# Kernel optimization log

Hardware: AMD Instinct MI355X
Metric: run time of the kernel (lower is better)

## Reference

```python
import jax, jax.numpy as jnp
import numpy as np

B, D = 256, 8                 # trees, tree depth (leaves at level D)
V, E, H = 32000, 128, 128     # vocab, embedding_dim, hidden_dim
N = 2 ** (D + 1) - 1          # 511 heap-indexed nodes per tree


def setup_inputs() -> dict:
    key = jax.random.key(0)
    ks = jax.random.split(key, 9)
    s = 0.05  # keep gate pre-activations in a sane range
    return {
        "tokens": jax.random.randint(ks[0], (B, N), 0, V),
        "arity": jax.random.randint(ks[1], (B, 2 ** D - 1), 0, 2).astype(jnp.int32),
        "emb": jax.random.normal(ks[2], (V, E), dtype=jnp.float32) * s,
        "W": jax.random.normal(ks[3], (4, E, H), dtype=jnp.float32) * s,      # i,f,o,u
        "bW": jax.random.normal(ks[4], (4, H), dtype=jnp.float32) * s,
        "Ubin": jax.random.normal(ks[5], (5, 2 * H, H), dtype=jnp.float32) * s,  # i,f_l,f_r,o,u
        "bUbin": jax.random.normal(ks[6], (5, H), dtype=jnp.float32) * s,
        "Uun": jax.random.normal(ks[7], (4, H, H), dtype=jnp.float32) * s,    # i,f,o,u
        "bUun": jax.random.normal(ks[8], (4, H), dtype=jnp.float32) * s,
    }


def reference(tokens, arity, emb, W, bW, Ubin, bUbin, Uun, bUun):
    # Level-synchronous bottom-up Tree-LSTM over heap-indexed perfect trees.
    x = emb[tokens]  # [B, N, E] embedding gather for every node
    depth = int(np.log2(tokens.shape[1] + 1)) - 1

    # Leaves (level `depth`): h = tanh(W_u x + b_u), c = 0
    off = 2 ** depth - 1
    lx = x[:, off:]  # [B, 2^D, E]
    h = jnp.tanh(jnp.einsum('bne,eh->bnh', lx, W[3]) + bW[3])
    c = jnp.zeros_like(h)

    for l in range(depth - 1, -1, -1):
        o2, cnt = 2 ** l - 1, 2 ** l
        nx = x[:, o2:o2 + cnt]            # [B, cnt, E] this level's tokens
        h_l, h_r = h[:, ::2], h[:, 1::2]   # children (heap order)
        c_l, c_r = c[:, ::2], c[:, 1::2]

        # Shared input projections for all 4 gates, fused into one GEMM
        Wx = jnp.einsum('bne,geh->gbnh', nx, W) + bW[:, None, None, :]
        hcat = jnp.concatenate([h_l, h_r], axis=-1)  # [B, cnt, 2H]
        Ub = jnp.einsum('bnk,gkh->gbnh', hcat, Ubin) + bUbin[:, None, None, :]
        Uu = jnp.einsum('bnh,gha->gbna', h_l, Uun) + bUun[:, None, None, :]

        # Binary branch: i, f_l, f_r (shared W_f), o, u
        i_b = jax.nn.sigmoid(Wx[0] + Ub[0])
        f_lg = jax.nn.sigmoid(Wx[1] + Ub[1])
        f_rg = jax.nn.sigmoid(Wx[1] + Ub[2])
        o_b = jax.nn.sigmoid(Wx[2] + Ub[3])
        u_b = jnp.tanh(Wx[3] + Ub[4])
        c_b = i_b * u_b + f_lg * c_l + f_rg * c_r
        h_b = o_b * jnp.tanh(c_b)

        # Unary branch (child = left child)
        i_u = jax.nn.sigmoid(Wx[0] + Uu[0])
        f_u = jax.nn.sigmoid(Wx[1] + Uu[1])
        o_u = jax.nn.sigmoid(Wx[2] + Uu[2])
        u_u = jnp.tanh(Wx[3] + Uu[3])
        c_u = i_u * u_u + f_u * c_l
        h_u = o_u * jnp.tanh(c_u)

        m = (arity[:, o2:o2 + cnt] == 1)[..., None]  # True -> binary node
        h = jnp.where(m, h_b, h_u)
        c = jnp.where(m, c_b, c_u)

    return h[:, 0], c[:, 0]  # root (h, c), each [B, H]
```

## Files before the change

### kernel.cpp

```cpp
#include <hip/hip_runtime.h>
#include <hip/hip_bf16.h>

#define NTOK 511
#define NINT 255

typedef unsigned short u16;
typedef __attribute__((ext_vector_type(8))) short bf16x8;
typedef __attribute__((ext_vector_type(4))) float f32x4;

constexpr int OFF_FLAG = 0;
constexpr int OFF_WB   = 4;
constexpr int W3B = 294912;
constexpr int WB_ELEMS = 311296;
constexpr int OFF_BIAS = OFF_WB + WB_ELEMS / 2;
constexpr int BW4 = 0, BUB4 = 512, BUB1 = 1024, BUU4 = 1152, B3 = 1664;
constexpr int BIAS_FLOATS = 1792;
constexpr int OFF_ROOT  = OFF_BIAS + BIAS_FLOATS;
constexpr int OFF_CHUNK = OFF_ROOT + 65536;
constexpr long PER_TREE = 49152;

__device__ __forceinline__ float bf2f(__hip_bfloat16 v) { return __bfloat162float(v); }
__device__ __forceinline__ short f2s(float f) {
    __hip_bfloat16 b = __float2bfloat16(f);
    return *reinterpret_cast<short*>(&b);
}
__device__ __forceinline__ float sigm(float x) { return 1.0f / (1.0f + __expf(-x)); }
__device__ __forceinline__ float tanh_(float x) { return 1.0f - 2.0f / (__expf(2.0f * x) + 1.0f); }

__device__ __forceinline__ float ldf(const void* p, long idx, int isbf) {
    return isbf ? bf2f(((const __hip_bfloat16*)p)[idx]) : ((const float*)p)[idx];
}

__device__ __forceinline__ bf16x8 ldA(const void* p, long idx, int isbf) {
    if (isbf) return *(const bf16x8*)((const short*)p + idx);
    const float* f = (const float*)p + idx;
    float4 a = *(const float4*)f, b = *(const float4*)(f + 4);
    bf16x8 r;
    r[0] = f2s(a.x); r[1] = f2s(a.y); r[2] = f2s(a.z); r[3] = f2s(a.w);
    r[4] = f2s(b.x); r[5] = f2s(b.y); r[6] = f2s(b.z); r[7] = f2s(b.w);
    return r;
}

typedef const __attribute__((address_space(1))) unsigned int* gp1_t;
typedef __attribute__((address_space(3))) unsigned int* lp3_t;
__device__ __forceinline__ void stage16(const void* g, void* l) {
    __builtin_amdgcn_global_load_lds((gp1_t)g, (lp3_t)l, 16, 0, 0);
}
__device__ __forceinline__ void stage36(const short* g, short* l, int t) {
#pragma unroll
    for (int s = 0; s < 9; ++s) {
        int off = (s * 256 + t) * 8;
        stage16(g + off, l + off);
    }
}

__global__ void detect_kernel(const void* W, float* ws) {
    if (threadIdx.x == 0 && blockIdx.x == 0) {
        const u16* u = (const u16*)W;
        int cnt = 0;
        for (int i = 0; i < 128; i += 2) {
            u16 x = u[i];
            int ex = (x >> 7) & 0xff;
            if (x == 0 || (ex >= 96 && ex <= 127)) cnt++;
        }
        ((int*)ws)[0] = (cnt >= 48) ? 1 : 0;
    }
}

__global__ __launch_bounds__(256) void repack_mfma(
    const void* W, const void* bW, const void* Ubin, const void* bUbin,
    const void* Uun, const void* bUun, float* ws)
{
    const int isbf = ((const int*)ws)[0];
    short* wb = (short*)(ws + OFF_WB);
    float* bias = ws + OFF_BIAS;
    int tid = blockIdx.x * blockDim.x + threadIdx.x;
    int nth = gridDim.x * blockDim.x;

    for (int idx = tid; idx < 294912; idx += nth) {
        int e = idx & 511, fjc = idx >> 9;
        int jc = fjc / 72, f = fjc - jc * 72;
        int lane = e >> 3, id8 = e & 7;
        int j = jc * 16 + (lane & 15);
        float v;
        if (f < 16) {
            int g = f >> 2, ks = f & 3;
            int k = ks * 32 + (lane >> 4) * 8 + id8;
            v = ldf(W, (long)g * 16384 + k * 128 + j, isbf);
        } else if (f < 32) {
            int fu = f - 16; int g = fu >> 2, ks = fu & 3;
            int k = ks * 32 + (lane >> 4) * 8 + id8;
            v = ldf(Uun, (long)g * 16384 + k * 128 + j, isbf);
        } else {
            int fb = f - 32; int g = fb >> 3, ks = fb & 7;
            int k = ks * 32 + (lane >> 4) * 8 + id8;
            v = ldf(Ubin, (long)g * 32768 + k * 128 + j, isbf);
        }
        wb[idx] = f2s(v);
    }
    for (int idx = tid; idx < 16384; idx += nth) {
        int e = idx & 511, frag = idx >> 9;
        int jc = frag >> 2, ks = frag & 3;
        int lane = e >> 3, id8 = e & 7;
        int k = ks * 32 + (lane >> 4) * 8 + id8;
        int j = jc * 16 + (lane & 15);
        wb[W3B + idx] = f2s(ldf(W, (long)3 * 16384 + k * 128 + j, isbf));
    }
    for (int j = tid; j < 128; j += nth) {
        float4 b;
        b.x = ldf(bW, 0 * 128 + j, isbf); b.y = ldf(bW, 1 * 128 + j, isbf);
        b.z = ldf(bW, 2 * 128 + j, isbf); b.w = ldf(bW, 3 * 128 + j, isbf);
        ((float4*)(bias + BW4))[j] = b;
        float4 bb;
        bb.x = ldf(bUbin, 0 * 128 + j, isbf); bb.y = ldf(bUbin, 1 * 128 + j, isbf);
        bb.z = ldf(bUbin, 2 * 128 + j, isbf); bb.w = ldf(bUbin, 3 * 128 + j, isbf);
        ((float4*)(bias + BUB4))[j] = bb;
        (bias + BUB1)[j] = ldf(bUbin, 4 * 128 + j, isbf);
        float4 bu;
        bu.x = ldf(bUun, 0 * 128 + j, isbf); bu.y = ldf(bUun, 1 * 128 + j, isbf);
        bu.z = ldf(bUun, 2 * 128 + j, isbf); bu.w = ldf(bUun, 3 * 128 + j, isbf);
        ((float4*)(bias + BUU4))[j] = bu;
        (bias + B3)[j] = ldf(bW, 3 * 128 + j, isbf);
    }
}

#define MFMA(A, B, C) __builtin_amdgcn_mfma_f32_16x16x32_bf16(A, B, C, 0, 0, 0)

__global__ __launch_bounds__(256, 2) void leaf_mfma(
    const int* __restrict__ tokens, const void* emb, const float* __restrict__ ws,
    short* __restrict__ hOut, int treeOff, int Mtot, int iters)
{
    __shared__ short hst[4][16][132];
    const int t = threadIdx.x;
    const int isbf = ((const int*)ws)[0];
    const int wv = t >> 6, lane = t & 63, quad = lane >> 4, l16 = lane & 15;
    const short* wb = (const short*)(ws + OFF_WB);
    const float* bias = ws + OFF_BIAS;

    bf16x8 bf[32];
#pragma unroll
    for (int f = 0; f < 32; ++f)
        bf[f] = *(const bf16x8*)(wb + W3B + f * 512 + lane * 8);
    float b3v[8];
#pragma unroll
    for (int jc = 0; jc < 8; ++jc) b3v[jc] = (bias + B3)[jc * 16 + l16];

    for (int it = 0; it < iters; ++it) {
        int rb = (blockIdx.x * iters + it) * 64 + wv * 16;
        if (rb >= Mtot) break;
        int p = rb + l16; if (p >= Mtot) p = Mtot - 1;
        int bl = p >> 8, i = p & 255;
        int tk = tokens[(long)(treeOff + bl) * NTOK + 255 + i];
        bf16x8 ax[4];
#pragma unroll
        for (int ks = 0; ks < 4; ++ks)
            ax[ks] = ldA(emb, (long)tk * 128 + ks * 32 + quad * 8, isbf);
        f32x4 acc[8];
#pragma unroll
        for (int jc = 0; jc < 8; ++jc) acc[jc] = {0.f, 0.f, 0.f, 0.f};
#pragma unroll
        for (int jc = 0; jc < 8; ++jc)
#pragma unroll
            for (int ks = 0; ks < 4; ++ks)
                acc[jc] = MFMA(ax[ks], bf[jc * 4 + ks], acc[jc]);
#pragma unroll
        for (int jc = 0; jc < 8; ++jc)
#pragma unroll
            for (int r = 0; r < 4; ++r)
                hst[wv][quad * 4 + r][jc * 16 + l16] = f2s(tanh_(acc[jc][r] + b3v[jc]));
        int nloc = lane >> 2, c0 = (lane & 3) * 4;
        int prow = rb + nloc;
        if (prow < Mtot) {
#pragma unroll
            for (int jcb = 0; jcb < 8; ++jcb) {
                uint2 v = *(const uint2*)&hst[wv][nloc][jcb * 16 + c0];
                *(uint2*)&hOut[((long)jcb * Mtot + prow) * 16 + c0] = v;
            }
        }
    }
}

template <int JCC, int MT>
__global__ __launch_bounds__(256, 2) void level_mfma(
    const int* __restrict__ tokens, const int* __restrict__ arity, const void* emb,
    const float* __restrict__ ws, const short* __restrict__ hChild,
    const float* __restrict__ cChild, short* __restrict__ hOut, float* __restrict__ cOut,
    float* __restrict__ rootH, float* __restrict__ rootC,
    int lvl, int treeOff, int leafchild, int isRoot, int Mtot, int Mchild, int NBM)
{
    __shared__ short Bs0[36 * 512];
    __shared__ short Bs1[36 * 512];
    __shared__ short hst[4][MT][16][20];
    __shared__ int tok[64 * MT];
    __shared__ int ar[64 * MT];

    constexpr int NODES = 64 * MT;
    const int t = threadIdx.x;
    const int isbf = ((const int*)ws)[0];
    const int jsx = blockIdx.x / NBM;
    const int mb  = blockIdx.x - jsx * NBM;
    const int jcLo = jsx * JCC;
    const int p0 = mb * NODES;
    const int wv = t >> 6, lane = t & 63, quad = lane >> 4, l16 = lane & 15;
    const int cnt = 1 << lvl, o2 = cnt - 1;
    const short* wb = (const short*)(ws + OFF_WB);
    const float* bias = ws + OFF_BIAS;

    if (t < NODES) {
        int p = p0 + t; if (p >= Mtot) p = Mtot - 1;
        int bl = p >> lvl, i = p - (bl << lvl);
        tok[t] = tokens[(long)(treeOff + bl) * NTOK + o2 + i];
        ar[t]  = arity[(long)(treeOff + bl) * NINT + o2 + i];
    }
    stage36(wb + (long)jcLo * 36864, Bs0, t);
    __syncthreads();

    bf16x8 ax[MT][4], ah[MT][8];
#pragma unroll
    for (int mt = 0; mt < MT; ++mt) {
        int row = wv * (16 * MT) + mt * 16 + l16;
        int p = p0 + row; if (p >= Mtot) p = Mtot - 1;
        int bl = p >> lvl, i = p - (bl << lvl);
        long crow = (long)bl * (cnt << 1) + 2 * i;
        int tk = tok[row];
#pragma unroll
        for (int ks = 0; ks < 4; ++ks)
            ax[mt][ks] = ldA(emb, (long)tk * 128 + ks * 32 + quad * 8, isbf);
#pragma unroll
        for (int ks = 0; ks < 8; ++ks) {
            int k0 = ks * 32 + quad * 8;
            int side = k0 >> 7, kl = k0 & 127;
            ah[mt][ks] = *(const bf16x8*)(hChild +
                ((long)(kl >> 4) * Mchild + crow + side) * 16 + (kl & 15));
        }
    }

    for (int jx = 0; jx < JCC; ++jx) {
        const int jc = jcLo + jx;
        const short* wj = wb + (long)jc * 36864;

        stage36(wj + 36 * 512, Bs1, t);

        float clv[MT][4], crv[MT][4];
#pragma unroll
        for (int mt = 0; mt < MT; ++mt)
#pragma unroll
        for (int r = 0; r < 4; ++r) {
            if (!leafchild) {
                int pe = p0 + wv * (16 * MT) + mt * 16 + quad * 4 + r;
                if (pe >= Mtot) pe = Mtot - 1;
                int ble = pe >> lvl, ie = pe - (ble << lvl);
                long crowe = (long)ble * (cnt << 1) + 2 * ie;
                clv[mt][r] = cChild[((long)jc * Mchild + crowe) * 16 + l16];
                crv[mt][r] = cChild[((long)jc * Mchild + crowe + 1) * 16 + l16];
            } else { clv[mt][r] = 0.f; crv[mt][r] = 0.f; }
        }

        const int j = jc * 16 + l16;
        const float4 bw = ((const float4*)(bias + BW4))[j];
        const float4 bb = ((const float4*)(bias + BUB4))[j];
        const float  b1 = (bias + BUB1)[j];
        const float4 bu = ((const float4*)(bias + BUU4))[j];

        f32x4 aW[4][MT], aU[4][MT], aB[5][MT];
#pragma unroll
        for (int g = 0; g < 4; ++g)
#pragma unroll
            for (int mt = 0; mt < MT; ++mt) { aW[g][mt] = {0,0,0,0}; aU[g][mt] = {0,0,0,0}; }
#pragma unroll
        for (int g = 0; g < 5; ++g)
#pragma unroll
            for (int mt = 0; mt < MT; ++mt) aB[g][mt] = {0,0,0,0};

#pragma unroll
        for (int f = 0; f < 16; ++f) {
            bf16x8 b = *(const bf16x8*)&Bs0[f * 512 + lane * 8];
#pragma unroll
            for (int mt = 0; mt < MT; ++mt)
                aW[f >> 2][mt] = MFMA(ax[mt][f & 3], b, aW[f >> 2][mt]);
        }
#pragma unroll
        for (int f = 16; f < 32; ++f) {
            bf16x8 b = *(const bf16x8*)&Bs0[f * 512 + lane * 8];
            int g = (f - 16) >> 2, ks = (f - 16) & 3;
#pragma unroll
            for (int mt = 0; mt < MT; ++mt)
                aU[g][mt] = MFMA(ah[mt][ks], b, aU[g][mt]);
        }
#pragma unroll
        for (int f = 32; f < 36; ++f) {
            bf16x8 b = *(const bf16x8*)&Bs0[f * 512 + lane * 8];
#pragma unroll
            for (int mt = 0; mt < MT; ++mt)
                aB[0][mt] = MFMA(ah[mt][f - 32], b, aB[0][mt]);
        }
        __syncthreads();

        if (jx + 1 < JCC)
            stage36(wj + 72 * 512, Bs0, t);

#pragma unroll
        for (int f = 36; f < 72; ++f) {
            bf16x8 b = *(const bf16x8*)&Bs1[(f - 36) * 512 + lane * 8];
            int fb = f - 32, g = fb >> 3, ks = fb & 7;
#pragma unroll
            for (int mt = 0; mt < MT; ++mt)
                aB[g][mt] = MFMA(ah[mt][ks], b, aB[g][mt]);
        }

#pragma unroll
        for (int mt = 0; mt < MT; ++mt) {
#pragma unroll
            for (int r = 0; r < 4; ++r) {
                int ml = wv * (16 * MT) + mt * 16 + quad * 4 + r;
                int p = p0 + ml;
                bool val = (p < Mtot);
                int pc = val ? p : Mtot - 1;
                int bl = pc >> lvl, i = pc - (bl << lvl);
                bool bin = (ar[ml] == 1);
                float w0 = aW[0][mt][r] + bw.x;
                float w1 = aW[1][mt][r] + bw.y;
                float w2 = aW[2][mt][r] + bw.z;
                float w3 = aW[3][mt][r] + bw.w;
                float pi, pf, po, pu;
                if (bin) { pi = w0 + aB[0][mt][r] + bb.x; pf = w1 + aB[1][mt][r] + bb.y;
                           po = w2 + aB[3][mt][r] + bb.w; pu = w3 + aB[4][mt][r] + b1; }
                else     { pi = w0 + aU[0][mt][r] + bu.x; pf = w1 + aU[1][mt][r] + bu.y;
                           po = w2 + aU[2][mt][r] + bu.z; pu = w3 + aU[3][mt][r] + bu.w; }
                float cl = clv[mt][r];
                float cr = bin ? crv[mt][r] : 0.f;
                float frv = bin ? sigm(w1 + aB[2][mt][r] + bb.z) : 0.f;
                float ig = sigm(pi), fg = sigm(pf), og = sigm(po), ug = tanh_(pu);
                float c = ig * ug + fg * cl + frv * cr;
                float h = og * tanh_(c);
                if (isRoot) {
                    if (val) {
                        rootH[(long)(treeOff + bl) * 128 + j] = h;
                        rootC[(long)(treeOff + bl) * 128 + j] = c;
                    }
                } else {
                    if (val) cOut[((long)jc * Mtot + pc) * 16 + l16] = c;
                    hst[wv][mt][quad * 4 + r][l16] = f2s(h);
                }
            }
        }
        if (!isRoot) {
            int nloc = lane >> 2, c0 = (lane & 3) * 4;
#pragma unroll
            for (int mt = 0; mt < MT; ++mt) {
                int prow = p0 + wv * (16 * MT) + mt * 16 + nloc;
                if (prow < Mtot) {
                    uint2 v = *(const uint2*)&hst[wv][mt][nloc][c0];
                    *(uint2*)&hOut[((long)jc * Mtot + prow) * 16 + c0] = v;
                }
            }
        }
        __syncthreads();
    }
}

__global__ __launch_bounds__(256) void out_kernel(const float* ws, void* out)
{
    const int isbf = ((const int*)ws)[0];
    const float* rootH = ws + OFF_ROOT;
    const float* rootC = rootH + 32768;
    int t = blockIdx.x * 256 + threadIdx.x;
    float h = rootH[t], c = rootC[t];
    if (isbf) {
        ((__hip_bfloat16*)out)[t]         = __float2bfloat16(h);
        ((__hip_bfloat16*)out)[32768 + t] = __float2bfloat16(c);
    } else {
        ((float*)out)[t]         = h;
        ((float*)out)[32768 + t] = c;
    }
}

extern "C" void kernel_launch(void* const* d_in, const int* in_sizes, int n_in,
                              void* d_out, int out_size, void* d_ws, size_t ws_size,
                              hipStream_t stream)
{
    const int* tokens = (const int*)d_in[0];
    const int* arity  = (const int*)d_in[1];
    const void* emb   = d_in[2];
    const void* W     = d_in[3];
    const void* bW    = d_in[4];
    const void* Ubin  = d_in[5];
    const void* bUbin = d_in[6];
    const void* Uun   = d_in[7];
    const void* bUun  = d_in[8];

    float* ws = (float*)d_ws;

    int Bc = 256;
    while (Bc > 1 && (size_t)(OFF_CHUNK + Bc * PER_TREE) * 4 > ws_size) Bc >>= 1;
    const int nCh = 256 / Bc;

    detect_kernel<<<1, 64, 0, stream>>>(W, ws);
    repack_mfma<<<128, 256, 0, stream>>>(W, bW, Ubin, bUbin, Uun, bUun, ws);

    short* Ha = (short*)(ws + OFF_CHUNK);
    short* Hb = Ha + (long)Bc * 32768;
    float* Ca = (float*)(Hb + (long)Bc * 16384);
    float* Cb = Ca + (long)Bc * 8192;
    float* rootH = ws + OFF_ROOT;
    float* rootC = rootH + 32768;

    for (int cidx = 0; cidx < nCh; ++cidx) {
        int toff = cidx * Bc;
        {
            int Mleaf = Bc * 256;
            int NBL = (Mleaf + 63) / 64; if (NBL > 512) NBL = 512;
            int itersL = (Mleaf + NBL * 64 - 1) / (NBL * 64);
            leaf_mfma<<<NBL, 256, 0, stream>>>(tokens, emb, ws, Ha, toff, Mleaf, itersL);
        }
        for (int l = 7; l >= 0; --l) {
            int M = Bc << l;
            int Mchild = Bc << (l + 1);
            const short* hC = (l & 1) ? Ha : Hb;
            const float* cC = (l & 1) ? Ca : Cb;
            short* hO = (l & 1) ? Hb : Ha;
            float* cO = (l & 1) ? Cb : Ca;
            int lc = (l == 7) ? 1 : 0;
            int isRoot = (l == 0) ? 1 : 0;
            if (l >= 5) {
                int Mb = (M + 127) / 128;
                int js = 1;
                while (js < 8 && Mb * js < 512) js <<= 1;
                int jcc = 8 / js;
                dim3 grid(Mb * js);
                if (jcc == 8)
                    level_mfma<8, 2><<<grid, 256, 0, stream>>>(tokens, arity, emb, ws, hC, cC, hO, cO,
                                                               rootH, rootC, l, toff, lc, isRoot, M, Mchild, Mb);
                else if (jcc == 4)
                    level_mfma<4, 2><<<grid, 256, 0, stream>>>(tokens, arity, emb, ws, hC, cC, hO, cO,
                                                               rootH, rootC, l, toff, lc, isRoot, M, Mchild, Mb);
                else if (jcc == 2)
                    level_mfma<2, 2><<<grid, 256, 0, stream>>>(tokens, arity, emb, ws, hC, cC, hO, cO,
                                                               rootH, rootC, l, toff, lc, isRoot, M, Mchild, Mb);
                else
                    level_mfma<1, 2><<<grid, 256, 0, stream>>>(tokens, arity, emb, ws, hC, cC, hO, cO,
                                                               rootH, rootC, l, toff, lc, isRoot, M, Mchild, Mb);
            } else {
                int Mb = (M + 63) / 64;
                dim3 grid(Mb * 8);
                level_mfma<1, 1><<<grid, 256, 0, stream>>>(tokens, arity, emb, ws, hC, cC, hO, cO,
                                                           rootH, rootC, l, toff, lc, isRoot, M, Mchild, Mb);
            }
        }
    }
    out_kernel<<<128, 256, 0, stream>>>(ws, d_out);
}
```

Baseline: 173.8 us.

## Keep one weight column-block resident per workgroup and loop over node tiles

The level kernel is restructured so each workgroup owns a single 16-column output block and stages that block's full 72-fragment weight slice into LDS once. It then loops over Q node tiles, reloading embeddings and child states per tile. Before, each workgroup held its node tile fixed and streamed weight blocks through double-buffered LDS with barriers between them. The change cuts repeated weight staging and the per-iteration syncs, and tokens and arity are now read directly from global memory. In exchange, activations are reloaded for every column block, the larger LDS footprint may lower occupancy, and weight staging no longer overlaps compute.

```diff
diff --git a/kernel.cpp b/kernel.cpp
--- a/kernel.cpp
+++ b/kernel.cpp
@@ -45,13 +45,6 @@
 typedef __attribute__((address_space(3))) unsigned int* lp3_t;
 __device__ __forceinline__ void stage16(const void* g, void* l) {
     __builtin_amdgcn_global_load_lds((gp1_t)g, (lp3_t)l, 16, 0, 0);
-}
-__device__ __forceinline__ void stage36(const short* g, short* l, int t) {
-#pragma unroll
-    for (int s = 0; s < 9; ++s) {
-        int off = (s * 256 + t) * 8;
-        stage16(g + off, l + off);
-    }
 }
 
 __global__ void detect_kernel(const void* W, float* ws) {
@@ -180,88 +173,84 @@
     }
 }
 
-template <int JCC, int MT>
-__global__ __launch_bounds__(256, 2) void level_mfma(
+template <int MT>
+__global__ __launch_bounds__(256, 2) void level2_mfma(
     const int* __restrict__ tokens, const int* __restrict__ arity, const void* emb,
     const float* __restrict__ ws, const short* __restrict__ hChild,
     const float* __restrict__ cChild, short* __restrict__ hOut, float* __restrict__ cOut,
     float* __restrict__ rootH, float* __restrict__ rootC,
-    int lvl, int treeOff, int leafchild, int isRoot, int Mtot, int Mchild, int NBM)
+    int lvl, int treeOff, int leafchild, int isRoot, int Mtot, int Mchild,
+    int NBMB, int Q)
 {
-    __shared__ short Bs0[36 * 512];
-    __shared__ short Bs1[36 * 512];
+    __shared__ short Bs[72 * 512];
     __shared__ short hst[4][MT][16][20];
-    __shared__ int tok[64 * MT];
-    __shared__ int ar[64 * MT];
 
     constexpr int NODES = 64 * MT;
     const int t = threadIdx.x;
     const int isbf = ((const int*)ws)[0];
-    const int jsx = blockIdx.x / NBM;
-    const int mb  = blockIdx.x - jsx * NBM;
-    const int jcLo = jsx * JCC;
-    const int p0 = mb * NODES;
+    const int jc = blockIdx.x / NBMB;
+    const int mb = blockIdx.x - jc * NBMB;
     const int wv = t >> 6, lane = t & 63, quad = lane >> 4, l16 = lane & 15;
     const int cnt = 1 << lvl, o2 = cnt - 1;
     const short* wb = (const short*)(ws + OFF_WB);
     const float* bias = ws + OFF_BIAS;
-
-    if (t < NODES) {
-        int p = p0 + t; if (p >= Mtot) p = Mtot - 1;
-        int bl = p >> lvl, i = p - (bl << lvl);
-        tok[t] = tokens[(long)(treeOff + bl) * NTOK + o2 + i];
-        ar[t]  = arity[(long)(treeOff + bl) * NINT + o2 + i];
-    }
-    stage36(wb + (long)jcLo * 36864, Bs0, t);
+    const short* wj = wb + (long)jc * 36864;
+
+#pragma unroll
+    for (int s = 0; s < 18; ++s) {
+        int off = (s * 256 + t) * 8;
+        stage16(wj + off, Bs + off);
+    }
+
+    const int j = jc * 16 + l16;
+    const float4 bw = ((const float4*)(bias + BW4))[j];
+    const float4 bb = ((const float4*)(bias + BUB4))[j];
+    const float  b1 = (bias + BUB1)[j];
+    const float4 bu = ((const float4*)(bias + BUU4))[j];
+
     __syncthreads();
 
-    bf16x8 ax[MT][4], ah[MT][8];
-#pragma unroll
-    for (int mt = 0; mt < MT; ++mt) {
-        int row = wv * (16 * MT) + mt * 16 + l16;
-        int p = p0 + row; if (p >= Mtot) p = Mtot - 1;
-        int bl = p >> lvl, i = p - (bl << lvl);
-        long crow = (long)bl * (cnt << 1) + 2 * i;
-        int tk = tok[row];
-#pragma unroll
-        for (int ks = 0; ks < 4; ++ks)
-            ax[mt][ks] = ldA(emb, (long)tk * 128 + ks * 32 + quad * 8, isbf);
-#pragma unroll
-        for (int ks = 0; ks < 8; ++ks) {
-            int k0 = ks * 32 + quad * 8;
-            int side = k0 >> 7, kl = k0 & 127;
-            ah[mt][ks] = *(const bf16x8*)(hChild +
-                ((long)(kl >> 4) * Mchild + crow + side) * 16 + (kl & 15));
-        }
-    }
-
-    for (int jx = 0; jx < JCC; ++jx) {
-        const int jc = jcLo + jx;
-        const short* wj = wb + (long)jc * 36864;
-
-        stage36(wj + 36 * 512, Bs1, t);
-
+    for (int q = 0; q < Q; ++q) {
+        const int p0 = (mb * Q + q) * NODES;
+        if (p0 >= Mtot) break;
+
+        bf16x8 ax[MT][4], ah[MT][8];
+#pragma unroll
+        for (int mt = 0; mt < MT; ++mt) {
+            int row = wv * (16 * MT) + mt * 16 + l16;
+            int p = p0 + row; if (p >= Mtot) p = Mtot - 1;
+            int bl = p >> lvl, i = p - (bl << lvl);
+            long crow = (long)bl * (cnt << 1) + 2 * i;
+            int tk = tokens[(long)(treeOff + bl) * NTOK + o2 + i];
+#pragma unroll
+            for (int ks = 0; ks < 4; ++ks)
+                ax[mt][ks] = ldA(emb, (long)tk * 128 + ks * 32 + quad * 8, isbf);
+#pragma unroll
+            for (int ks = 0; ks < 8; ++ks) {
+                int k0 = ks * 32 + quad * 8;
+                int side = k0 >> 7, kl = k0 & 127;
+                ah[mt][ks] = *(const bf16x8*)(hChild +
+                    ((long)(kl >> 4) * Mchild + crow + side) * 16 + (kl & 15));
+            }
+        }
+
+        int arv[MT][4];
         float clv[MT][4], crv[MT][4];
 #pragma unroll
         for (int mt = 0; mt < MT; ++mt)
 #pragma unroll
         for (int r = 0; r < 4; ++r) {
+            int pe = p0 + wv * (16 * MT) + mt * 16 + quad * 4 + r;
+            if (pe >= Mtot) pe = Mtot - 1;
+            int ble = pe >> lvl, ie = pe - (ble << lvl);
+            arv[mt][r] = arity[(long)(treeOff + ble) * NINT + o2 + ie];
             if (!leafchild) {
-                int pe = p0 + wv * (16 * MT) + mt * 16 + quad * 4 + r;
-                if (pe >= Mtot) pe = Mtot - 1;
-                int ble = pe >> lvl, ie = pe - (ble << lvl);
                 long crowe = (long)ble * (cnt << 1) + 2 * ie;
                 clv[mt][r] = cChild[((long)jc * Mchild + crowe) * 16 + l16];
                 crv[mt][r] = cChild[((long)jc * Mchild + crowe + 1) * 16 + l16];
             } else { clv[mt][r] = 0.f; crv[mt][r] = 0.f; }
         }
 
-        const int j = jc * 16 + l16;
-        const float4 bw = ((const float4*)(bias + BW4))[j];
-        const float4 bb = ((const float4*)(bias + BUB4))[j];
-        const float  b1 = (bias + BUB1)[j];
-        const float4 bu = ((const float4*)(bias + BUU4))[j];
-
         f32x4 aW[4][MT], aU[4][MT], aB[5][MT];
 #pragma unroll
         for (int g = 0; g < 4; ++g)
@@ -274,34 +263,22 @@
 
 #pragma unroll
         for (int f = 0; f < 16; ++f) {
-            bf16x8 b = *(const bf16x8*)&Bs0[f * 512 + lane * 8];
+            bf16x8 b = *(const bf16x8*)&Bs[f * 512 + lane * 8];
 #pragma unroll
             for (int mt = 0; mt < MT; ++mt)
                 aW[f >> 2][mt] = MFMA(ax[mt][f & 3], b, aW[f >> 2][mt]);
         }
 #pragma unroll
         for (int f = 16; f < 32; ++f) {
-            bf16x8 b = *(const bf16x8*)&Bs0[f * 512 + lane * 8];
+            bf16x8 b = *(const bf16x8*)&Bs[f * 512 + lane * 8];
             int g = (f - 16) >> 2, ks = (f - 16) & 3;
 #pragma unroll
             for (int mt = 0; mt < MT; ++mt)
                 aU[g][mt] = MFMA(ah[mt][ks], b, aU[g][mt]);
         }
 #pragma unroll
-        for (int f = 32; f < 36; ++f) {
-            bf16x8 b = *(const bf16x8*)&Bs0[f * 512 + lane * 8];
-#pragma unroll
-            for (int mt = 0; mt < MT; ++mt)
-                aB[0][mt] = MFMA(ah[mt][f - 32], b, aB[0][mt]);
-        }
-        __syncthreads();
-
-        if (jx + 1 < JCC)
-            stage36(wj + 72 * 512, Bs0, t);
-
-#pragma unroll
-        for (int f = 36; f < 72; ++f) {
-            bf16x8 b = *(const bf16x8*)&Bs1[(f - 36) * 512 + lane * 8];
+        for (int f = 32; f < 72; ++f) {
+            bf16x8 b = *(const bf16x8*)&Bs[f * 512 + lane * 8];
             int fb = f - 32, g = fb >> 3, ks = fb & 7;
 #pragma unroll
             for (int mt = 0; mt < MT; ++mt)
@@ -316,8 +293,8 @@
                 int p = p0 + ml;
                 bool val = (p < Mtot);
                 int pc = val ? p : Mtot - 1;
-                int bl = pc >> lvl, i = pc - (bl << lvl);
-                bool bin = (ar[ml] == 1);
+                int bl = pc >> lvl;
+                bool bin = (arv[mt][r] == 1);
                 float w0 = aW[0][mt][r] + bw.x;
                 float w1 = aW[1][mt][r] + bw.y;
                 float w2 = aW[2][mt][r] + bw.z;
@@ -355,7 +332,6 @@
                 }
             }
         }
-        __syncthreads();
     }
 }
 
@@ -423,28 +399,17 @@
             int lc = (l == 7) ? 1 : 0;
             int isRoot = (l == 0) ? 1 : 0;
             if (l >= 5) {
-                int Mb = (M + 127) / 128;
-                int js = 1;
-                while (js < 8 && Mb * js < 512) js <<= 1;
-                int jcc = 8 / js;
-                dim3 grid(Mb * js);
-                if (jcc == 8)
-                    level_mfma<8, 2><<<grid, 256, 0, stream>>>(tokens, arity, emb, ws, hC, cC, hO, cO,
-                                                               rootH, rootC, l, toff, lc, isRoot, M, Mchild, Mb);
-                else if (jcc == 4)
-                    level_mfma<4, 2><<<grid, 256, 0, stream>>>(tokens, arity, emb, ws, hC, cC, hO, cO,
-                                                               rootH, rootC, l, toff, lc, isRoot, M, Mchild, Mb);
-                else if (jcc == 2)
-                    level_mfma<2, 2><<<grid, 256, 0, stream>>>(tokens, arity, emb, ws, hC, cC, hO, cO,
-                                                               rootH, rootC, l, toff, lc, isRoot, M, Mchild, Mb);
-                else
-                    level_mfma<1, 2><<<grid, 256, 0, stream>>>(tokens, arity, emb, ws, hC, cC, hO, cO,
-                                                               rootH, rootC, l, toff, lc, isRoot, M, Mchild, Mb);
+                int NBM = (M + 127) / 128;
+                int Q = (NBM + 63) / 64;
+                int NBMB = (NBM + Q - 1) / Q;
+                level2_mfma<2><<<dim3(NBMB * 8), 256, 0, stream>>>(
+                    tokens, arity, emb, ws, hC, cC, hO, cO, rootH, rootC,
+                    l, toff, lc, isRoot, M, Mchild, NBMB, Q);
             } else {
-                int Mb = (M + 63) / 64;
-                dim3 grid(Mb * 8);
-                level_mfma<1, 1><<<grid, 256, 0, stream>>>(tokens, arity, emb, ws, hC, cC, hO, cO,
-                                                           rootH, rootC, l, toff, lc, isRoot, M, Mchild, Mb);
+                int NBM = (M + 63) / 64;
+                level2_mfma<1><<<dim3(NBM * 8), 256, 0, stream>>>(
+                    tokens, arity, emb, ws, hC, cC, hO, cO, rootH, rootC,
+                    l, toff, lc, isRoot, M, Mchild, NBM, 1);
             }
         }
     }
```

Result: faster. 164.8 us (-5.2%).
